# Performance work log

Measured on AMD Instinct MI355X. Metric: run time of the kernel, lower is better.

Reference implementation:

```python
import jax, jax.numpy as jnp
import numpy as np

B, T, D_MODEL, D_HIDDEN, MAX_SEQLEN = 4, 2048, 1024, 1024, 2048


def setup_inputs() -> dict:
    key = jax.random.key(0)
    ks = jax.random.split(key, 8)
    scale = 0.02  # keep exp() and linear outputs in a sane range
    return {
        "q": jax.random.normal(ks[0], (B, T, D_MODEL), dtype=jnp.float32),
        "k": jax.random.normal(ks[1], (B, T, D_MODEL), dtype=jnp.float32),
        "v": jax.random.normal(ks[2], (B, T, D_MODEL), dtype=jnp.float32),
        "Wq": jax.random.normal(ks[3], (D_HIDDEN, D_MODEL), dtype=jnp.float32) * scale,
        "Wk": jax.random.normal(ks[4], (D_HIDDEN, D_MODEL), dtype=jnp.float32) * scale,
        "Wv": jax.random.normal(ks[5], (D_HIDDEN, D_MODEL), dtype=jnp.float32) * scale,
        "Wo": jax.random.normal(ks[6], (D_MODEL, D_HIDDEN), dtype=jnp.float32) * scale,
        "W_bias": jax.random.normal(ks[7], (MAX_SEQLEN, MAX_SEQLEN), dtype=jnp.float32) * scale,
    }


def reference(q, k, v, Wq, Wk, Wv, Wo, W_bias):
    Ti = q.shape[1]
    Tj = k.shape[1]
    # Linear projections (torch Linear: x @ W.T), bias=False
    Q = jnp.einsum('btm,hm->bth', q, Wq)
    K = jnp.einsum('btm,hm->bth', k, Wk)
    V = jnp.einsum('btm,hm->bth', v, Wv)
    pos_bias = W_bias[:Ti, :Tj][None]              # (1, Ti, Tj)
    # Faithful to original: max over dim 0 (batch dim for K, singleton dim for pos_bias)
    max_key = jnp.max(K, axis=0, keepdims=True)    # (1, Tj, Dh)
    max_pos_bias = jnp.max(pos_bias, axis=0, keepdims=True)  # == pos_bias (dim 0 is size 1)
    exp_key = jnp.exp(K - max_key)                 # (B, Tj, Dh)
    exp_pos_bias = jnp.exp(pos_bias - max_pos_bias)  # all-ones, kept for faithfulness
    num = jnp.einsum('bij,bjd->bid', exp_pos_bias, exp_key * V)
    den = jnp.einsum('bij,bjd->bid', exp_pos_bias, exp_key)
    Yt = jax.nn.sigmoid(Q) * num / den             # (B, Ti, Dh)
    return jnp.einsum('bth,mh->btm', Yt, Wo)
```

## Files before the change

### kernel.cpp

```cpp
#include <hip/hip_runtime.h>
#include <hip/hip_bf16.h>

typedef __bf16 bf16;
typedef __bf16 bf16x8 __attribute__((ext_vector_type(8)));
typedef __bf16 bf16x4 __attribute__((ext_vector_type(4)));
typedef float f32x4 __attribute__((ext_vector_type(4)));

#define B_   4
#define T_   2048
#define DM_  1024
#define DH_  1024
#define MROWS (B_ * T_)

struct CvtJob { const float* src; bf16* dst; int nf4; };
struct CvtArgs { CvtJob job[6]; };

__global__ __launch_bounds__(256) void cvt_kernel(CvtArgs args) {
  CvtJob jb = args.job[blockIdx.y];
  int f4 = blockIdx.x * 1024 + threadIdx.x * 2;
  if (f4 >= jb.nf4) return;
  const float4* s = (const float4*)jb.src;
  float4 a0 = s[f4];
  float4 a1 = s[f4 + 1];
  float4 b0 = s[f4 + 512];
  float4 b1 = s[f4 + 513];
  bf16x8 oa, ob;
  oa[0] = (bf16)a0.x; oa[1] = (bf16)a0.y; oa[2] = (bf16)a0.z; oa[3] = (bf16)a0.w;
  oa[4] = (bf16)a1.x; oa[5] = (bf16)a1.y; oa[6] = (bf16)a1.z; oa[7] = (bf16)a1.w;
  ob[0] = (bf16)b0.x; ob[1] = (bf16)b0.y; ob[2] = (bf16)b0.z; ob[3] = (bf16)b0.w;
  ob[4] = (bf16)b1.x; ob[5] = (bf16)b1.y; ob[6] = (bf16)b1.z; ob[7] = (bf16)b1.w;
  *(bf16x8*)(jb.dst + (size_t)f4 * 4) = oa;
  *(bf16x8*)(jb.dst + (size_t)(f4 + 512) * 4) = ob;
}

struct GemmJob { const bf16* A; const bf16* Bw; float* Cf; bf16* Cb; };
struct GemmArgs { GemmJob job[4]; int N; int K; };

__global__ __launch_bounds__(256) void gemm_bt(GemmArgs ga) {
  const GemmJob jb = ga.job[blockIdx.z];
  const int N = ga.N, K = ga.K;
  __shared__ bf16 As[128 * 64];
  __shared__ bf16 Bs[128 * 64];

  const int tid  = threadIdx.x;
  const int lane = tid & 63;
  const int wave = tid >> 6;
  const int wm   = (wave >> 1) * 64;
  const int wn   = (wave & 1) * 64;
  const int tileM = blockIdx.y * 128;
  const int tileN = blockIdx.x * 128;

  f32x4 acc[4][4] = {};

  const int sr = lane >> 3;
  const int sc = (lane & 7) ^ sr;

  for (int k0 = 0; k0 < K; k0 += 64) {
#pragma unroll
    for (int l = 0; l < 4; ++l) {
      int grp = wave * 4 + l;
      int row = grp * 8 + sr;
      const bf16* gaadr = jb.A + (size_t)(tileM + row) * K + k0 + sc * 8;
      __builtin_amdgcn_global_load_lds(
          (const __attribute__((address_space(1))) void*)gaadr,
          (__attribute__((address_space(3))) void*)&As[grp * 512], 16, 0, 0);
      const bf16* gbadr = jb.Bw + (size_t)(tileN + row) * K + k0 + sc * 8;
      __builtin_amdgcn_global_load_lds(
          (const __attribute__((address_space(1))) void*)gbadr,
          (__attribute__((address_space(3))) void*)&Bs[grp * 512], 16, 0, 0);
    }
    __syncthreads();

    const int quad = lane >> 4;
#pragma unroll
    for (int s = 0; s < 2; ++s) {
      bf16x8 af[4], bfr[4];
#pragma unroll
      for (int mt = 0; mt < 4; ++mt) {
        int row = wm + mt * 16 + (lane & 15);
        int chunk = (s * 4 + quad) ^ (row & 7);
        af[mt] = *(const bf16x8*)&As[row * 64 + chunk * 8];
      }
#pragma unroll
      for (int nt = 0; nt < 4; ++nt) {
        int row = wn + nt * 16 + (lane & 15);
        int chunk = (s * 4 + quad) ^ (row & 7);
        bfr[nt] = *(const bf16x8*)&Bs[row * 64 + chunk * 8];
      }
#pragma unroll
      for (int mt = 0; mt < 4; ++mt)
#pragma unroll
        for (int nt = 0; nt < 4; ++nt)
          acc[mt][nt] = __builtin_amdgcn_mfma_f32_16x16x32_bf16(
              af[mt], bfr[nt], acc[mt][nt], 0, 0, 0);
    }
    __syncthreads();
  }

  const int cn = lane & 15;
  const int cr = (lane >> 4) * 4;
  if (jb.Cf) {
#pragma unroll
    for (int mt = 0; mt < 4; ++mt)
#pragma unroll
      for (int nt = 0; nt < 4; ++nt)
#pragma unroll
        for (int r = 0; r < 4; ++r) {
          int row = tileM + wm + mt * 16 + cr + r;
          int col = tileN + wn + nt * 16 + cn;
          jb.Cf[(size_t)row * N + col] = acc[mt][nt][r];
        }
  } else {
#pragma unroll
    for (int mt = 0; mt < 4; ++mt)
#pragma unroll
      for (int nt = 0; nt < 4; ++nt)
#pragma unroll
        for (int r = 0; r < 4; ++r) {
          int row = tileM + wm + mt * 16 + cr + r;
          int col = tileN + wn + nt * 16 + cn;
          float sv = 1.f / (1.f + __expf(-acc[mt][nt][r]));
          jb.Cb[(size_t)row * N + col] = (bf16)sv;
        }
  }
}

__global__ __launch_bounds__(256) void reduce_kv(
    const float* __restrict__ Kf, const float* __restrict__ Vf,
    float* __restrict__ num, float* __restrict__ den) {
  const int d  = blockIdx.x * 256 + threadIdx.x;
  const int j0 = blockIdx.y * 32;
  const size_t bs = (size_t)T_ * DH_;
  float n0 = 0, n1 = 0, n2 = 0, n3 = 0, e0 = 0, e1 = 0, e2 = 0, e3 = 0;
#pragma unroll 2
  for (int j = j0; j < j0 + 32; ++j) {
    size_t off = (size_t)j * DH_ + d;
    float k0 = Kf[off], k1 = Kf[off + bs], k2 = Kf[off + 2 * bs], k3 = Kf[off + 3 * bs];
    float v0 = Vf[off], v1 = Vf[off + bs], v2 = Vf[off + 2 * bs], v3 = Vf[off + 3 * bs];
    float m = fmaxf(fmaxf(k0, k1), fmaxf(k2, k3));
    float w0 = __expf(k0 - m), w1 = __expf(k1 - m);
    float w2 = __expf(k2 - m), w3 = __expf(k3 - m);
    e0 += w0; e1 += w1; e2 += w2; e3 += w3;
    n0 += w0 * v0; n1 += w1 * v1; n2 += w2 * v2; n3 += w3 * v3;
  }
  atomicAdd(&num[0 * DH_ + d], n0);
  atomicAdd(&num[1 * DH_ + d], n1);
  atomicAdd(&num[2 * DH_ + d], n2);
  atomicAdd(&num[3 * DH_ + d], n3);
  atomicAdd(&den[0 * DH_ + d], e0);
  atomicAdd(&den[1 * DH_ + d], e1);
  atomicAdd(&den[2 * DH_ + d], e2);
  atomicAdd(&den[3 * DH_ + d], e3);
}

__global__ __launch_bounds__(256) void scale_wo(
    const float* __restrict__ Wo, const float* __restrict__ num,
    const float* __restrict__ den, bf16* __restrict__ Wos) {
  int i = (blockIdx.x * 256 + threadIdx.x) * 4;
  int h = i & (DH_ - 1);
  float4 w = *(const float4*)(Wo + i);
#pragma unroll
  for (int b = 0; b < 4; ++b) {
    float4 nu = *(const float4*)(num + b * DH_ + h);
    float4 de = *(const float4*)(den + b * DH_ + h);
    bf16x4 o;
    o[0] = (bf16)(w.x * nu.x / de.x);
    o[1] = (bf16)(w.y * nu.y / de.y);
    o[2] = (bf16)(w.z * nu.z / de.z);
    o[3] = (bf16)(w.w * nu.w / de.w);
    *(bf16x4*)(Wos + (size_t)b * DH_ * DM_ + i) = o;
  }
}

extern "C" void kernel_launch(void* const* d_in, const int* in_sizes, int n_in,
                              void* d_out, int out_size, void* d_ws, size_t ws_size,
                              hipStream_t stream) {
  const float* q  = (const float*)d_in[0];
  const float* k  = (const float*)d_in[1];
  const float* v  = (const float*)d_in[2];
  const float* Wq = (const float*)d_in[3];
  const float* Wk = (const float*)d_in[4];
  const float* Wv = (const float*)d_in[5];
  const float* Wo = (const float*)d_in[6];
  float* out = (float*)d_out;

  char* ws = (char*)d_ws;
  size_t off = 0;
  auto alloc = [&](size_t bytes) {
    char* p = ws + off;
    off += (bytes + 255) & ~(size_t)255;
    return p;
  };
  const size_t actN = (size_t)MROWS * DM_;
  const size_t wN   = (size_t)DH_ * DM_;

  bf16* qb  = (bf16*)alloc(actN * 2);
  bf16* kb  = (bf16*)alloc(actN * 2);
  bf16* vb  = (bf16*)alloc(actN * 2);
  bf16* Wqb = (bf16*)alloc(wN * 2);
  bf16* Wkb = (bf16*)alloc(wN * 2);
  bf16* Wvb = (bf16*)alloc(wN * 2);
  float* Kf = (float*)alloc(actN * 4);
  float* Vf = (float*)alloc(actN * 4);
  bf16* Yb  = (bf16*)alloc(actN * 2);
  bf16* Wos = (bf16*)alloc(4 * wN * 2);
  float* num = (float*)alloc(B_ * DH_ * 4);
  float* den = (float*)alloc(B_ * DH_ * 4);

  CvtArgs ca;
  ca.job[0] = {q,  qb,  (int)(actN / 4)};
  ca.job[1] = {k,  kb,  (int)(actN / 4)};
  ca.job[2] = {v,  vb,  (int)(actN / 4)};
  ca.job[3] = {Wq, Wqb, (int)(wN / 4)};
  ca.job[4] = {Wk, Wkb, (int)(wN / 4)};
  ca.job[5] = {Wv, Wvb, (int)(wN / 4)};
  cvt_kernel<<<dim3(actN / 4 / 1024, 6), 256, 0, stream>>>(ca);

  hipMemsetAsync(num, 0, 2 * B_ * DH_ * sizeof(float), stream);

  GemmArgs g1;
  g1.N = DH_; g1.K = DM_;
  g1.job[0] = {kb, Wkb, Kf, nullptr};
  g1.job[1] = {vb, Wvb, Vf, nullptr};
  g1.job[2] = {qb, Wqb, nullptr, Yb};
  g1.job[3] = {nullptr, nullptr, nullptr, nullptr};
  gemm_bt<<<dim3(DH_ / 128, MROWS / 128, 3), 256, 0, stream>>>(g1);

  reduce_kv<<<dim3(4, 64), 256, 0, stream>>>(Kf, Vf, num, den);

  scale_wo<<<dim3(wN / 4 / 256), 256, 0, stream>>>(Wo, num, den, Wos);

  GemmArgs g2;
  g2.N = DM_; g2.K = DH_;
  for (int b = 0; b < 4; ++b)
    g2.job[b] = {Yb + (size_t)b * T_ * DH_, Wos + (size_t)b * wN,
                 out + (size_t)b * T_ * DM_, nullptr};
  gemm_bt<<<dim3(DM_ / 128, T_ / 128, 4), 256, 0, stream>>>(g2);
}
```

Before: 290.8 us.

## Fuse fp32-to-bf16 activation conversion into projection GEMM and store K/V as bf16

The projection GEMM now loads the fp32 q/k/v activations directly, converts them to bf16 in registers and writes them to LDS. This removes the separate conversion pass and its bf16 intermediate buffers. K and V projections are stored as bf16 instead of fp32, which halves the traffic the reduce_kv kernel reads; that kernel is reworked to process two columns per thread. Block indices are remapped so tiles are grouped by XCD for L2 locality. The trade-off is that A-tile loads go through registers instead of direct global-to-LDS copies, and K/V lose precision.

```diff
diff --git a/kernel.cpp b/kernel.cpp
--- a/kernel.cpp
+++ b/kernel.cpp
@@ -4,6 +4,7 @@
 typedef __bf16 bf16;
 typedef __bf16 bf16x8 __attribute__((ext_vector_type(8)));
 typedef __bf16 bf16x4 __attribute__((ext_vector_type(4)));
+typedef __bf16 bf16x2 __attribute__((ext_vector_type(2)));
 typedef float f32x4 __attribute__((ext_vector_type(4)));
 
 #define B_   4
@@ -13,7 +14,7 @@
 #define MROWS (B_ * T_)
 
 struct CvtJob { const float* src; bf16* dst; int nf4; };
-struct CvtArgs { CvtJob job[6]; };
+struct CvtArgs { CvtJob job[3]; };
 
 __global__ __launch_bounds__(256) void cvt_kernel(CvtArgs args) {
   CvtJob jb = args.job[blockIdx.y];
@@ -33,9 +34,10 @@
   *(bf16x8*)(jb.dst + (size_t)(f4 + 512) * 4) = ob;
 }
 
-struct GemmJob { const bf16* A; const bf16* Bw; float* Cf; bf16* Cb; };
+struct GemmJob { const void* A; const bf16* Bw; float* Cf; bf16* Cb; int mode; };
 struct GemmArgs { GemmJob job[4]; int N; int K; };
 
+template <bool AF32>
 __global__ __launch_bounds__(256) void gemm_bt(GemmArgs ga) {
   const GemmJob jb = ga.job[blockIdx.z];
   const int N = ga.N, K = ga.K;
@@ -47,8 +49,14 @@
   const int wave = tid >> 6;
   const int wm   = (wave >> 1) * 64;
   const int wn   = (wave & 1) * 64;
-  const int tileM = blockIdx.y * 128;
-  const int tileN = blockIdx.x * 128;
+
+  const int f   = blockIdx.y * 8 + blockIdx.x;
+  const int xcd = f & 7;
+  const int j   = f >> 3;
+  const int bn  = j & 7;
+  const int bm  = (j >> 3) * 8 + xcd;
+  const int tileM = bm * 128;
+  const int tileN = bn * 128;
 
   f32x4 acc[4][4] = {};
 
@@ -56,14 +64,43 @@
   const int sc = (lane & 7) ^ sr;
 
   for (int k0 = 0; k0 < K; k0 += 64) {
+    if (AF32) {
+      const float* Af = (const float*)jb.A;
+      float4 av[4][2];
+#pragma unroll
+      for (int l = 0; l < 4; ++l) {
+        int grp = wave * 4 + l;
+        int row = grp * 8 + sr;
+        const float4* ga4 = (const float4*)(Af + (size_t)(tileM + row) * K + k0 + sc * 8);
+        av[l][0] = ga4[0];
+        av[l][1] = ga4[1];
+      }
+#pragma unroll
+      for (int l = 0; l < 4; ++l) {
+        int grp = wave * 4 + l;
+        bf16x8 w;
+        w[0] = (bf16)av[l][0].x; w[1] = (bf16)av[l][0].y;
+        w[2] = (bf16)av[l][0].z; w[3] = (bf16)av[l][0].w;
+        w[4] = (bf16)av[l][1].x; w[5] = (bf16)av[l][1].y;
+        w[6] = (bf16)av[l][1].z; w[7] = (bf16)av[l][1].w;
+        *(bf16x8*)&As[grp * 512 + lane * 8] = w;
+      }
+    } else {
+      const bf16* Ab = (const bf16*)jb.A;
+#pragma unroll
+      for (int l = 0; l < 4; ++l) {
+        int grp = wave * 4 + l;
+        int row = grp * 8 + sr;
+        const bf16* gaadr = Ab + (size_t)(tileM + row) * K + k0 + sc * 8;
+        __builtin_amdgcn_global_load_lds(
+            (const __attribute__((address_space(1))) void*)gaadr,
+            (__attribute__((address_space(3))) void*)&As[grp * 512], 16, 0, 0);
+      }
+    }
 #pragma unroll
     for (int l = 0; l < 4; ++l) {
       int grp = wave * 4 + l;
       int row = grp * 8 + sr;
-      const bf16* gaadr = jb.A + (size_t)(tileM + row) * K + k0 + sc * 8;
-      __builtin_amdgcn_global_load_lds(
-          (const __attribute__((address_space(1))) void*)gaadr,
-          (__attribute__((address_space(3))) void*)&As[grp * 512], 16, 0, 0);
       const bf16* gbadr = jb.Bw + (size_t)(tileN + row) * K + k0 + sc * 8;
       __builtin_amdgcn_global_load_lds(
           (const __attribute__((address_space(1))) void*)gbadr,
@@ -99,7 +136,7 @@
 
   const int cn = lane & 15;
   const int cr = (lane >> 4) * 4;
-  if (jb.Cf) {
+  if (jb.mode == 0) {
 #pragma unroll
     for (int mt = 0; mt < 4; ++mt)
 #pragma unroll
@@ -110,7 +147,7 @@
           int col = tileN + wn + nt * 16 + cn;
           jb.Cf[(size_t)row * N + col] = acc[mt][nt][r];
         }
-  } else {
+  } else if (jb.mode == 1) {
 #pragma unroll
     for (int mt = 0; mt < 4; ++mt)
 #pragma unroll
@@ -119,38 +156,58 @@
         for (int r = 0; r < 4; ++r) {
           int row = tileM + wm + mt * 16 + cr + r;
           int col = tileN + wn + nt * 16 + cn;
-          float sv = 1.f / (1.f + __expf(-acc[mt][nt][r]));
-          jb.Cb[(size_t)row * N + col] = (bf16)sv;
+          jb.Cb[(size_t)row * N + col] =
+              (bf16)(1.f / (1.f + __expf(-acc[mt][nt][r])));
         }
+  } else {
+#pragma unroll
+    for (int mt = 0; mt < 4; ++mt)
+#pragma unroll
+      for (int nt = 0; nt < 4; ++nt)
+#pragma unroll
+        for (int r = 0; r < 4; ++r) {
+          int row = tileM + wm + mt * 16 + cr + r;
+          int col = tileN + wn + nt * 16 + cn;
+          jb.Cb[(size_t)row * N + col] = (bf16)acc[mt][nt][r];
+        }
   }
 }
 
 __global__ __launch_bounds__(256) void reduce_kv(
-    const float* __restrict__ Kf, const float* __restrict__ Vf,
+    const bf16* __restrict__ Kb, const bf16* __restrict__ Vb,
     float* __restrict__ num, float* __restrict__ den) {
-  const int d  = blockIdx.x * 256 + threadIdx.x;
-  const int j0 = blockIdx.y * 32;
+  const int d  = (blockIdx.x * 256 + threadIdx.x) * 2;
+  const int j0 = blockIdx.y * 16;
   const size_t bs = (size_t)T_ * DH_;
-  float n0 = 0, n1 = 0, n2 = 0, n3 = 0, e0 = 0, e1 = 0, e2 = 0, e3 = 0;
-#pragma unroll 2
-  for (int j = j0; j < j0 + 32; ++j) {
-    size_t off = (size_t)j * DH_ + d;
-    float k0 = Kf[off], k1 = Kf[off + bs], k2 = Kf[off + 2 * bs], k3 = Kf[off + 3 * bs];
-    float v0 = Vf[off], v1 = Vf[off + bs], v2 = Vf[off + 2 * bs], v3 = Vf[off + 3 * bs];
-    float m = fmaxf(fmaxf(k0, k1), fmaxf(k2, k3));
-    float w0 = __expf(k0 - m), w1 = __expf(k1 - m);
-    float w2 = __expf(k2 - m), w3 = __expf(k3 - m);
-    e0 += w0; e1 += w1; e2 += w2; e3 += w3;
-    n0 += w0 * v0; n1 += w1 * v1; n2 += w2 * v2; n3 += w3 * v3;
-  }
-  atomicAdd(&num[0 * DH_ + d], n0);
-  atomicAdd(&num[1 * DH_ + d], n1);
-  atomicAdd(&num[2 * DH_ + d], n2);
-  atomicAdd(&num[3 * DH_ + d], n3);
-  atomicAdd(&den[0 * DH_ + d], e0);
-  atomicAdd(&den[1 * DH_ + d], e1);
-  atomicAdd(&den[2 * DH_ + d], e2);
-  atomicAdd(&den[3 * DH_ + d], e3);
+  float n[4][2] = {}, e[4][2] = {};
+  for (int jj = j0; jj < j0 + 16; ++jj) {
+    size_t off = (size_t)jj * DH_ + d;
+    float kf[4][2], vf[4][2];
+#pragma unroll
+    for (int b = 0; b < 4; ++b) {
+      bf16x2 kk = *(const bf16x2*)(Kb + off + b * bs);
+      bf16x2 vv = *(const bf16x2*)(Vb + off + b * bs);
+      kf[b][0] = (float)kk[0]; kf[b][1] = (float)kk[1];
+      vf[b][0] = (float)vv[0]; vf[b][1] = (float)vv[1];
+    }
+#pragma unroll
+    for (int c = 0; c < 2; ++c) {
+      float m = fmaxf(fmaxf(kf[0][c], kf[1][c]), fmaxf(kf[2][c], kf[3][c]));
+#pragma unroll
+      for (int b = 0; b < 4; ++b) {
+        float w = __expf(kf[b][c] - m);
+        e[b][c] += w;
+        n[b][c] += w * vf[b][c];
+      }
+    }
+  }
+#pragma unroll
+  for (int b = 0; b < 4; ++b)
+#pragma unroll
+    for (int c = 0; c < 2; ++c) {
+      atomicAdd(&num[b * DH_ + d + c], n[b][c]);
+      atomicAdd(&den[b * DH_ + d + c], e[b][c]);
+    }
 }
 
 __global__ __launch_bounds__(256) void scale_wo(
@@ -194,39 +251,33 @@
   const size_t actN = (size_t)MROWS * DM_;
   const size_t wN   = (size_t)DH_ * DM_;
 
-  bf16* qb  = (bf16*)alloc(actN * 2);
-  bf16* kb  = (bf16*)alloc(actN * 2);
-  bf16* vb  = (bf16*)alloc(actN * 2);
   bf16* Wqb = (bf16*)alloc(wN * 2);
   bf16* Wkb = (bf16*)alloc(wN * 2);
   bf16* Wvb = (bf16*)alloc(wN * 2);
-  float* Kf = (float*)alloc(actN * 4);
-  float* Vf = (float*)alloc(actN * 4);
+  bf16* Kb  = (bf16*)alloc(actN * 2);
+  bf16* Vb  = (bf16*)alloc(actN * 2);
   bf16* Yb  = (bf16*)alloc(actN * 2);
   bf16* Wos = (bf16*)alloc(4 * wN * 2);
   float* num = (float*)alloc(B_ * DH_ * 4);
   float* den = (float*)alloc(B_ * DH_ * 4);
 
   CvtArgs ca;
-  ca.job[0] = {q,  qb,  (int)(actN / 4)};
-  ca.job[1] = {k,  kb,  (int)(actN / 4)};
-  ca.job[2] = {v,  vb,  (int)(actN / 4)};
-  ca.job[3] = {Wq, Wqb, (int)(wN / 4)};
-  ca.job[4] = {Wk, Wkb, (int)(wN / 4)};
-  ca.job[5] = {Wv, Wvb, (int)(wN / 4)};
-  cvt_kernel<<<dim3(actN / 4 / 1024, 6), 256, 0, stream>>>(ca);
+  ca.job[0] = {Wq, Wqb, (int)(wN / 4)};
+  ca.job[1] = {Wk, Wkb, (int)(wN / 4)};
+  ca.job[2] = {Wv, Wvb, (int)(wN / 4)};
+  cvt_kernel<<<dim3(wN / 4 / 1024, 3), 256, 0, stream>>>(ca);
 
   hipMemsetAsync(num, 0, 2 * B_ * DH_ * sizeof(float), stream);
 
   GemmArgs g1;
   g1.N = DH_; g1.K = DM_;
-  g1.job[0] = {kb, Wkb, Kf, nullptr};
-  g1.job[1] = {vb, Wvb, Vf, nullptr};
-  g1.job[2] = {qb, Wqb, nullptr, Yb};
-  g1.job[3] = {nullptr, nullptr, nullptr, nullptr};
-  gemm_bt<<<dim3(DH_ / 128, MROWS / 128, 3), 256, 0, stream>>>(g1);
-
-  reduce_kv<<<dim3(4, 64), 256, 0, stream>>>(Kf, Vf, num, den);
+  g1.job[0] = {k, Wkb, nullptr, Kb, 2};
+  g1.job[1] = {v, Wvb, nullptr, Vb, 2};
+  g1.job[2] = {q, Wqb, nullptr, Yb, 1};
+  g1.job[3] = {nullptr, nullptr, nullptr, nullptr, 0};
+  gemm_bt<true><<<dim3(8, MROWS / 128, 3), 256, 0, stream>>>(g1);
+
+  reduce_kv<<<dim3(2, 128), 256, 0, stream>>>(Kb, Vb, num, den);
 
   scale_wo<<<dim3(wN / 4 / 256), 256, 0, stream>>>(Wo, num, den, Wos);
 
@@ -234,6 +285,6 @@
   g2.N = DM_; g2.K = DH_;
   for (int b = 0; b < 4; ++b)
     g2.job[b] = {Yb + (size_t)b * T_ * DH_, Wos + (size_t)b * wN,
-                 out + (size_t)b * T_ * DM_, nullptr};
-  gemm_bt<<<dim3(DM_ / 128, T_ / 128, 4), 256, 0, stream>>>(g2);
-}
+                 out + (size_t)b * T_ * DM_, nullptr, 0};
+  gemm_bt<false><<<dim3(8, T_ / 128, 4), 256, 0, stream>>>(g2);
+}
```

New measurement: 295.3 us. No clear change (+1.6%).
